# Performance work log

Hardware: AMD Instinct MI355X
Metric: run time of the kernel (lower is better)

## Reference

```python
import jax, jax.numpy as jnp
import numpy as np

BATCH = 8192
IN_F = 1024
OUT_F = 1024
GRID_SIZE = 5
SPLINE_ORDER = 3
GRID_LO, GRID_HI = -1.0, 1.0


def setup_inputs() -> dict:
    key = jax.random.key(0)
    k1, k2, k3, k4 = jax.random.split(key, 4)
    x = jax.random.normal(k1, (BATCH, IN_F), dtype=jnp.float32)
    # grid buffer: extended knot vector, same for every input feature
    h = (GRID_HI - GRID_LO) / GRID_SIZE
    knots = jnp.linspace(GRID_LO - SPLINE_ORDER * h, GRID_HI + SPLINE_ORDER * h,
                         GRID_SIZE + 2 * SPLINE_ORDER + 1, dtype=jnp.float32)
    grid = jnp.tile(knots[None, :], (IN_F, 1))  # [in, 12]
    fan_in_scale = 1.0 / np.sqrt(IN_F)
    base_weight = jax.random.normal(k2, (OUT_F, IN_F), dtype=jnp.float32) * fan_in_scale
    spline_weight = jax.random.normal(k3, (IN_F, GRID_SIZE + SPLINE_ORDER, OUT_F), dtype=jnp.float32) * 0.1
    spline_scaler = jax.random.normal(k4, (IN_F, OUT_F), dtype=jnp.float32) * fan_in_scale
    return {"x": x, "grid": grid, "base_weight": base_weight,
            "spline_weight": spline_weight, "spline_scaler": spline_scaler}


def b_splines(x, grid):
    """Cox-de Boor recursion. x: [B, in], grid: [in, G+2k+1] -> [B, in, G+k]."""
    xe = x[:, :, None]  # [B, in, 1]
    bases = ((xe >= grid[:, :-1]) & (xe < grid[:, 1:])).astype(x.dtype)  # [B, in, G+2k]
    for k in range(1, SPLINE_ORDER + 1):
        left = (xe - grid[:, :-(k + 1)]) / (grid[:, k:-1] - grid[:, :-(k + 1)])
        right = (grid[:, k + 1:] - xe) / (grid[:, k + 1:] - grid[:, 1:-k])
        bases = left * bases[:, :, :-1] + right * bases[:, :, 1:]
    return bases  # [B, in, G+k]


def reference(x, grid, base_weight, spline_weight, spline_scaler):
    # base branch: SiLU(x) @ W_base^T
    base_out = jax.nn.silu(x) @ base_weight.T  # [B, out]
    # spline branch
    basis = b_splines(x, grid)  # [B, in, G+k]
    scaled_w = spline_weight * spline_scaler[:, None, :]  # [in, G+k, out]
    spline_out = jnp.einsum('bik,iko->bo', basis, scaled_w)  # [B, out]
    return base_out + spline_out
```

## Files before the change

kernel.cpp:

```cpp
#include <hip/hip_runtime.h>
#include <cstdint>
#include <cstddef>

#define BATCH 8192
#define IN_F 1024
#define OUT_F 1024
#define NSPL 9
#define KDIM (IN_F * NSPL)

#define BM 256
#define BN 128
#define BK 64
#define NTILE (KDIM / BK)

typedef __bf16 bf16x8 __attribute__((ext_vector_type(8)));
typedef float f32x4 __attribute__((ext_vector_type(4)));

__device__ __forceinline__ void g2l16(const void* g, void* l) {
  __builtin_amdgcn_global_load_lds(
      (__attribute__((address_space(1))) void*)(g),
      (__attribute__((address_space(3))) void*)(l),
      16, 0, 0);
}

__device__ __forceinline__ void barrier_raw() {
  asm volatile("" ::: "memory");
  __builtin_amdgcn_s_barrier();
  asm volatile("" ::: "memory");
}

__global__ void build_w(const float* __restrict__ bw, const float* __restrict__ sw,
                        const float* __restrict__ sc, __bf16* __restrict__ Wt) {
  __shared__ float s_sw[16 * 8 * 64];
  __shared__ float s_sc[16 * 64];
  __shared__ float s_bw[64 * 16];
  const int tid = threadIdx.x;
  const int o0 = (blockIdx.x & 15) * 64;
  const int i0 = (blockIdx.x >> 4) * 16;

#pragma unroll
  for (int it = 0; it < 32; ++it) {
    const int t = it * 256 + tid;
    const int i = t >> 9, r = (t >> 6) & 7, oo = t & 63;
    s_sw[t] = sw[((size_t)(i0 + i) * 8 + r) * OUT_F + o0 + oo];
  }
#pragma unroll
  for (int it = 0; it < 4; ++it) {
    const int t = it * 256 + tid;
    const int i = t >> 6, oo = t & 63;
    s_sc[t] = sc[(size_t)(i0 + i) * OUT_F + o0 + oo];
  }
#pragma unroll
  for (int it = 0; it < 4; ++it) {
    const int t = it * 256 + tid;
    const int oo = t >> 4, ii = t & 15;
    s_bw[t] = bw[(size_t)(o0 + oo) * IN_F + i0 + ii];
  }
  __syncthreads();

  const int oo = tid >> 2;
  const int isub = (tid & 3) * 4;
#pragma unroll
  for (int is = 0; is < 4; ++is) {
    const int i = isub + is;
    __bf16* dst = Wt + (size_t)(o0 + oo) * KDIM + (size_t)(i0 + i) * NSPL;
    dst[0] = (__bf16)s_bw[oo * 16 + i];
    const float scal = s_sc[i * 64 + oo];
#pragma unroll
    for (int r = 0; r < 8; ++r)
      dst[1 + r] = (__bf16)(s_sw[i * 512 + r * 64 + oo] * scal);
  }
}

__global__ void build_a(const float* __restrict__ x, __bf16* __restrict__ A) {
  __shared__ __align__(16) __bf16 rowbuf[KDIM];
  const int b = blockIdx.x;
  const int tid = threadIdx.x;
#pragma unroll
  for (int c = 0; c < IN_F / 256; ++c) {
    const int i = c * 256 + tid;
    const float v = x[(size_t)b * IN_F + i];
    float w[NSPL];
#pragma unroll
    for (int r = 0; r < NSPL; ++r) w[r] = 0.f;
    w[0] = v / (1.f + __expf(-v));
    const float p = (v + 2.2f) * 2.5f;
    const int cell = (int)floorf(p);
    if (cell >= 0 && cell <= 10 && v < 2.2f) {
      const float t = p - (float)cell;
      const float t2 = t * t, t3 = t2 * t;
      const float omt = 1.f - t;
      const float b0 = (1.f / 6.f) * omt * omt * omt;
      const float b1 = (1.f / 6.f) * (3.f * t3 - 6.f * t2 + 4.f);
      const float b2 = (1.f / 6.f) * (-3.f * t3 + 3.f * t2 + 3.f * t + 1.f);
      const float b3 = (1.f / 6.f) * t3;
      const int j0 = cell - 3;
      if (j0 + 0 >= 0 && j0 + 0 <= 7) w[1 + j0 + 0] = b0;
      if (j0 + 1 >= 0 && j0 + 1 <= 7) w[1 + j0 + 1] = b1;
      if (j0 + 2 >= 0 && j0 + 2 <= 7) w[1 + j0 + 2] = b2;
      if (j0 + 3 >= 0 && j0 + 3 <= 7) w[1 + j0 + 3] = b3;
    }
    __bf16* d = rowbuf + (size_t)i * NSPL;
#pragma unroll
    for (int r = 0; r < NSPL; ++r) d[r] = (__bf16)w[r];
  }
  __syncthreads();
  const uint4* src = (const uint4*)rowbuf;
  uint4* dst = (uint4*)(A + (size_t)b * KDIM);
  for (int t = tid; t < KDIM * 2 / 16; t += 256)
    dst[t] = src[t];
}

__global__ __launch_bounds__(512, 2) void gemm_bt(const __bf16* __restrict__ A,
                                                  const __bf16* __restrict__ W,
                                                  float* __restrict__ out) {
  __shared__ __align__(16) __bf16 As[3][BM * BK];
  __shared__ __align__(16) __bf16 Bs[3][BN * BK];

  const int tid = threadIdx.x;
  const int wv = tid >> 6;
  const int lane = tid & 63;

  const int bid = blockIdx.x;
  const int swz = (bid & 7) * 32 + (bid >> 3);
  const int m0 = (swz & 31) * BM;
  const int n0 = (swz >> 5) * BN;

  const int wr = wv >> 1;
  const int wc = wv & 1;

  const int srow = lane >> 3;
  const int usrc = (lane & 7) ^ srow;
  const __bf16* gA = A + (size_t)(m0 + wv * 32 + srow) * KDIM + usrc * 8;
  const __bf16* gB = W + (size_t)(n0 + wv * 16 + srow) * KDIM + usrc * 8;

#define STAGE3_FIRST(q, tt)                                          \
  do {                                                               \
    const size_t ko = (size_t)(tt) * BK;                             \
    g2l16(gA + ko,                      &As[q][(wv * 32 + 0) * BK]); \
    g2l16(gA + ko + 8 * (size_t)KDIM,   &As[q][(wv * 32 + 8) * BK]); \
    g2l16(gB + ko,                      &Bs[q][(wv * 16 + 0) * BK]); \
  } while (0)
#define STAGE3_SECOND(q, tt)                                          \
  do {                                                                \
    const size_t ko = (size_t)(tt) * BK;                              \
    g2l16(gA + ko + 16 * (size_t)KDIM, &As[q][(wv * 32 + 16) * BK]);  \
    g2l16(gA + ko + 24 * (size_t)KDIM, &As[q][(wv * 32 + 24) * BK]);  \
    g2l16(gB + ko + 8 * (size_t)KDIM,  &Bs[q][(wv * 16 + 8) * BK]);   \
  } while (0)

  const int mrow = lane & 15;
  const int quad = lane >> 4;
  int aoff[4], boff[4];
#pragma unroll
  for (int mt = 0; mt < 4; ++mt) aoff[mt] = (wr * 64 + mt * 16 + mrow) * BK;
#pragma unroll
  for (int nt = 0; nt < 4; ++nt) boff[nt] = (wc * 64 + nt * 16 + mrow) * BK;
  const int colx0 = ((quad) ^ (mrow & 7)) * 8;
  const int colx1 = ((4 + quad) ^ (mrow & 7)) * 8;

  f32x4 acc[4][4];
  const f32x4 zero = {0.f, 0.f, 0.f, 0.f};
#pragma unroll
  for (int mt = 0; mt < 4; ++mt)
#pragma unroll
    for (int nt = 0; nt < 4; ++nt) acc[mt][nt] = zero;

  STAGE3_FIRST(0, 0);
  STAGE3_SECOND(0, 0);
  STAGE3_FIRST(1, 1);
  STAGE3_SECOND(1, 1);
  asm volatile("s_waitcnt vmcnt(6)" ::: "memory");
  barrier_raw();

  int q = 0;
  for (int t = 0; t < NTILE; ++t) {
    const int qp = (q == 0) ? 2 : q - 1;

    bf16x8 a0[4], b0[4];
#pragma unroll
    for (int mt = 0; mt < 4; ++mt) a0[mt] = *(const bf16x8*)(&As[q][aoff[mt] + colx0]);
#pragma unroll
    for (int nt = 0; nt < 4; ++nt) b0[nt] = *(const bf16x8*)(&Bs[q][boff[nt] + colx0]);
    if (t + 2 < NTILE) STAGE3_FIRST(qp, t + 2);
    barrier_raw();
    __builtin_amdgcn_s_setprio(1);
#pragma unroll
    for (int mt = 0; mt < 4; ++mt)
#pragma unroll
      for (int nt = 0; nt < 4; ++nt)
        acc[mt][nt] = __builtin_amdgcn_mfma_f32_16x16x32_bf16(a0[mt], b0[nt],
                                                              acc[mt][nt], 0, 0, 0);
    __builtin_amdgcn_s_setprio(0);
    barrier_raw();

    bf16x8 a1[4], b1[4];
#pragma unroll
    for (int mt = 0; mt < 4; ++mt) a1[mt] = *(const bf16x8*)(&As[q][aoff[mt] + colx1]);
#pragma unroll
    for (int nt = 0; nt < 4; ++nt) b1[nt] = *(const bf16x8*)(&Bs[q][boff[nt] + colx1]);
    if (t + 2 < NTILE) {
      STAGE3_SECOND(qp, t + 2);
      asm volatile("s_waitcnt vmcnt(6)" ::: "memory");
    } else {
      asm volatile("s_waitcnt vmcnt(0)" ::: "memory");
    }
    barrier_raw();
    __builtin_amdgcn_s_setprio(1);
#pragma unroll
    for (int mt = 0; mt < 4; ++mt)
#pragma unroll
      for (int nt = 0; nt < 4; ++nt)
        acc[mt][nt] = __builtin_amdgcn_mfma_f32_16x16x32_bf16(a1[mt], b1[nt],
                                                              acc[mt][nt], 0, 0, 0);
    __builtin_amdgcn_s_setprio(0);
    barrier_raw();

    q = (q == 2) ? 0 : q + 1;
  }

#pragma unroll
  for (int mt = 0; mt < 4; ++mt) {
#pragma unroll
    for (int nt = 0; nt < 4; ++nt) {
      const int col = n0 + wc * 64 + nt * 16 + mrow;
      const int rbase = m0 + wr * 64 + mt * 16 + quad * 4;
#pragma unroll
      for (int r = 0; r < 4; ++r)
        out[(size_t)(rbase + r) * OUT_F + col] = acc[mt][nt][r];
    }
  }
#undef STAGE3_FIRST
#undef STAGE3_SECOND
}

extern "C" void kernel_launch(void* const* d_in, const int* in_sizes, int n_in,
                              void* d_out, int out_size, void* d_ws, size_t ws_size,
                              hipStream_t stream) {
  const float* x  = (const float*)d_in[0];
  const float* bw = (const float*)d_in[2];
  const float* sw = (const float*)d_in[3];
  const float* sc = (const float*)d_in[4];
  float* out = (float*)d_out;

  __bf16* Wt = (__bf16*)d_ws;
  __bf16* Ab = (__bf16*)((char*)d_ws +
                         (size_t)OUT_F * KDIM * sizeof(__bf16));

  build_w<<<1024, 256, 0, stream>>>(bw, sw, sc, Wt);
  build_a<<<BATCH, 256, 0, stream>>>(x, Ab);
  gemm_bt<<<(BATCH / BM) * (OUT_F / BN), 512, 0, stream>>>(Ab, Wt, out);
}
```

Measured before the change: 319.3 us.

## Vectorize basis build per thread and remap GEMM tiles for XCD locality

build_a now handles two batch rows per block. Each thread loads 8 contiguous inputs as float4, computes branch-free spline bases into a register union, and writes 16-byte LDS stores, cutting scalar bf16 LDS writes and the launch count. The GEMM block-to-tile mapping is also changed so that each XCD owns four adjacent M tiles across all N tiles, which is meant to improve L2 reuse of A rows within a chiplet. The branch-free selects add some ALU work per feature.

Measured after the change: 289.5 us. 9.3% less time.

```diff
diff --git a/kernel.cpp b/kernel.cpp
--- a/kernel.cpp
+++ b/kernel.cpp
@@ -72,43 +72,58 @@
   }
 }
 
-__global__ void build_a(const float* __restrict__ x, __bf16* __restrict__ A) {
-  __shared__ __align__(16) __bf16 rowbuf[KDIM];
-  const int b = blockIdx.x;
+__global__ __launch_bounds__(256) void build_a(const float* __restrict__ x,
+                                               __bf16* __restrict__ A) {
+  __shared__ __align__(16) __bf16 rowbuf[2 * KDIM];
   const int tid = threadIdx.x;
-#pragma unroll
-  for (int c = 0; c < IN_F / 256; ++c) {
-    const int i = c * 256 + tid;
-    const float v = x[(size_t)b * IN_F + i];
-    float w[NSPL];
-#pragma unroll
-    for (int r = 0; r < NSPL; ++r) w[r] = 0.f;
-    w[0] = v / (1.f + __expf(-v));
+  const int r2 = tid >> 7;
+  const int tr = tid & 127;
+  const size_t b = (size_t)blockIdx.x * 2 + r2;
+
+  const float4* xp = (const float4*)(x + b * IN_F + (size_t)tr * 8);
+  const float4 v0 = xp[0], v1 = xp[1];
+  const float vv[8] = {v0.x, v0.y, v0.z, v0.w, v1.x, v1.y, v1.z, v1.w};
+
+  union HB { __bf16 h[72]; uint4 q[9]; } hb;
+
+#pragma unroll
+  for (int f = 0; f < 8; ++f) {
+    const float v = vv[f];
+    const float s0 = v / (1.f + __expf(-v));
     const float p = (v + 2.2f) * 2.5f;
     const int cell = (int)floorf(p);
-    if (cell >= 0 && cell <= 10 && v < 2.2f) {
-      const float t = p - (float)cell;
-      const float t2 = t * t, t3 = t2 * t;
-      const float omt = 1.f - t;
-      const float b0 = (1.f / 6.f) * omt * omt * omt;
-      const float b1 = (1.f / 6.f) * (3.f * t3 - 6.f * t2 + 4.f);
-      const float b2 = (1.f / 6.f) * (-3.f * t3 + 3.f * t2 + 3.f * t + 1.f);
-      const float b3 = (1.f / 6.f) * t3;
-      const int j0 = cell - 3;
-      if (j0 + 0 >= 0 && j0 + 0 <= 7) w[1 + j0 + 0] = b0;
-      if (j0 + 1 >= 0 && j0 + 1 <= 7) w[1 + j0 + 1] = b1;
-      if (j0 + 2 >= 0 && j0 + 2 <= 7) w[1 + j0 + 2] = b2;
-      if (j0 + 3 >= 0 && j0 + 3 <= 7) w[1 + j0 + 3] = b3;
+    const bool ok = (cell >= 0) && (cell <= 10) && (v < 2.2f);
+    const float gate = ok ? (1.f / 6.f) : 0.f;
+    const float t = p - (float)cell;
+    const float t2 = t * t, t3 = t2 * t;
+    const float omt = 1.f - t;
+    const float c0 = gate * omt * omt * omt;
+    const float c1 = gate * (3.f * t3 - 6.f * t2 + 4.f);
+    const float c2 = gate * (-3.f * t3 + 3.f * t2 + 3.f * t + 1.f);
+    const float c3 = gate * t3;
+    const int j0 = cell - 3;
+    hb.h[f * 9 + 0] = (__bf16)s0;
+#pragma unroll
+    for (int r = 0; r < 8; ++r) {
+      const int d = r - j0;
+      float val = (d == 0) ? c0 : 0.f;
+      val = (d == 1) ? c1 : val;
+      val = (d == 2) ? c2 : val;
+      val = (d == 3) ? c3 : val;
+      hb.h[f * 9 + 1 + r] = (__bf16)val;
     }
-    __bf16* d = rowbuf + (size_t)i * NSPL;
-#pragma unroll
-    for (int r = 0; r < NSPL; ++r) d[r] = (__bf16)w[r];
-  }
+  }
+
+  uint4* ldst = (uint4*)(rowbuf + (size_t)r2 * KDIM) + (size_t)tr * 9;
+#pragma unroll
+  for (int k = 0; k < 9; ++k) ldst[k] = hb.q[k];
   __syncthreads();
+
   const uint4* src = (const uint4*)rowbuf;
-  uint4* dst = (uint4*)(A + (size_t)b * KDIM);
-  for (int t = tid; t < KDIM * 2 / 16; t += 256)
-    dst[t] = src[t];
+  uint4* dst = (uint4*)(A + (size_t)blockIdx.x * 2 * KDIM);
+#pragma unroll
+  for (int it = 0; it < 9; ++it)
+    dst[it * 256 + tid] = src[it * 256 + tid];
 }
 
 __global__ __launch_bounds__(512, 2) void gemm_bt(const __bf16* __restrict__ A,
@@ -122,9 +137,10 @@
   const int lane = tid & 63;
 
   const int bid = blockIdx.x;
-  const int swz = (bid & 7) * 32 + (bid >> 3);
-  const int m0 = (swz & 31) * BM;
-  const int n0 = (swz >> 5) * BN;
+  const int xcd = bid & 7;
+  const int j = bid >> 3;
+  const int m0 = (xcd * 4 + (j & 3)) * BM;
+  const int n0 = (j >> 2) * BN;
 
   const int wr = wv >> 1;
   const int wc = wv & 1;
@@ -248,6 +264,6 @@
                          (size_t)OUT_F * KDIM * sizeof(__bf16));
 
   build_w<<<1024, 256, 0, stream>>>(bw, sw, sc, Wt);
-  build_a<<<BATCH, 256, 0, stream>>>(x, Ab);
+  build_a<<<BATCH / 2, 256, 0, stream>>>(x, Ab);
   gemm_bt<<<(BATCH / BM) * (OUT_F / BN), 512, 0, stream>>>(Ab, Wt, out);
 }
```
